# Kernel optimization log

Hardware: AMD Instinct MI355X
Metric: run time of the kernel (lower is better)

Reference implementation:

```python
import jax, jax.numpy as jnp
import numpy as np


def setup_inputs() -> dict:
    key = jax.random.key(0)
    k1, k2 = jax.random.split(key)
    C, N = 64, 500000
    src = jax.random.normal(k1, (C, N), dtype=jnp.float32)
    index = jax.random.randint(k2, (N,), 0, N, dtype=jnp.int64)
    return {"src": src, "index": index}


def reference(src, index):
    # scatter_max(src, index, dim=-1, out=src):
    #   out[c, k] = max(src[c, k], max_{j: index[j]==k} src[c, j])
    #   argmax[c, k] = source position j achieving the segment max
    #                  (sentinel N if the segment is empty / never updated)
    C, N = src.shape
    index = index.astype(jnp.int32)
    # Segment max over the point axis; empty segments get -inf.
    seg_max = jax.ops.segment_max(src.T, index, num_segments=N).T  # [C, N]
    out = jnp.maximum(src, seg_max)
    # argmax: smallest source position whose value equals the segment max.
    pos = jnp.arange(N, dtype=jnp.int32)
    is_max = src == seg_max[:, index]                       # [C, N]
    cand = jnp.where(is_max, pos[None, :], N).astype(jnp.int32)
    arg_min = jax.ops.segment_min(cand.T, index, num_segments=N).T  # [C, N]
    argmax = jnp.where(seg_max >= src, arg_min, N).astype(jnp.int32)
    return out, argmax
```

## Files before the change

kernel.cpp:

```cpp
#include <hip/hip_runtime.h>
#include <stdint.h>

typedef unsigned int u32;
typedef unsigned long long u64;

__device__ __forceinline__ u32 f2o(float f) {
    u32 u = __float_as_uint(f);
    return (u & 0x80000000u) ? ~u : (u | 0x80000000u);
}
__device__ __forceinline__ float o2f(u32 u) {
    return __uint_as_float((u & 0x80000000u) ? (u & 0x7fffffffu) : ~u);
}

#define TJ 64

__global__ __launch_bounds__(256) void scatter_tr_kernel(
        const float* __restrict__ src, const int* __restrict__ index,
        u64* __restrict__ packt, int N, int vec_ok) {
    __shared__ float tile[64 * 65];
    __shared__ int idx[TJ];
    const int j0 = blockIdx.x * TJ;
    const int t = threadIdx.x;
    const int nj = min(TJ, N - j0);

    if (t < nj) idx[t] = index[j0 + t];

    if (nj == TJ && vec_ok) {
        const int r0 = t >> 4, q = t & 15;
        #pragma unroll
        for (int p = 0; p < 4; ++p) {
            const int c = r0 + p * 16;
            float4 v = *reinterpret_cast<const float4*>(src + (size_t)c * N + j0 + q * 4);
            float* d = &tile[c * 65 + q * 4];
            d[0] = v.x; d[1] = v.y; d[2] = v.z; d[3] = v.w;
        }
    } else {
        for (int e = t; e < 64 * TJ; e += 256) {
            const int c = e >> 6, jj = e & 63;
            tile[c * 65 + jj] = (jj < nj) ? src[(size_t)c * N + j0 + jj] : 0.0f;
        }
    }
    __syncthreads();

    const int lane = t & 63, w = t >> 6;
    #pragma unroll 4
    for (int jj = w; jj < nj; jj += 4) {
        const int j = j0 + jj;
        const u32 k = (u32)idx[jj];
        const float v = tile[lane * 65 + jj];
        const u64 p = ((u64)f2o(v) << 32) | (u32)(~(u32)j);
        atomicMax(&packt[(size_t)k * 64 + lane], p);
    }
}

__global__ __launch_bounds__(256) void finalize_tr_kernel(
        const float* __restrict__ src, const u64* __restrict__ packt,
        float* __restrict__ outv, float* __restrict__ outa, int N, u32 NV) {
    __shared__ u32 lord[64 * 65];
    __shared__ u32 larg[64 * 65];
    const int k0 = blockIdx.x * 64;
    const int t = threadIdx.x;
    const int nk = min(64, N - k0);

    {
        const u64* base = packt + (size_t)k0 * 64;
        const int npairs = nk * 32;
        #pragma unroll
        for (int v = 0; v < 8; ++v) {
            const int i2 = t + v * 256;
            if (i2 < npairs) {
                const int e = i2 * 2;
                ulonglong2 p = *reinterpret_cast<const ulonglong2*>(base + e);
                const int kk = e >> 6, c = e & 63;
                lord[kk * 65 + c]     = (u32)(p.x >> 32);
                larg[kk * 65 + c]     = ~(u32)p.x;
                lord[kk * 65 + c + 1] = (u32)(p.y >> 32);
                larg[kk * 65 + c + 1] = ~(u32)p.y;
            }
        }
    }
    __syncthreads();

    const int lane = t & 63, w = t >> 6;
    const int q = lane & 15, cg = lane >> 4;
    const int kq = q * 4;
    #pragma unroll
    for (int p = 0; p < 4; ++p) {
        const int c = p * 16 + w * 4 + cg;
        const size_t off = (size_t)c * N + k0 + kq;
        if (kq + 3 < nk) {
            float4 s = *reinterpret_cast<const float4*>(src + off);
            float sv[4] = {s.x, s.y, s.z, s.w};
            float4 ov, av;
            float* po = &ov.x; float* pa = &av.x;
            #pragma unroll
            for (int i = 0; i < 4; ++i) {
                const u32 ord = lord[(kq + i) * 65 + c];
                float o, a;
                if (ord == 0u) { o = sv[i]; a = (float)NV; }
                else {
                    const float m = o2f(ord);
                    o = fmaxf(sv[i], m);
                    a = (m >= sv[i]) ? (float)larg[(kq + i) * 65 + c] : (float)NV;
                }
                po[i] = o; pa[i] = a;
            }
            *reinterpret_cast<float4*>(outv + off) = ov;
            *reinterpret_cast<float4*>(outa + off) = av;
        } else {
            for (int i = 0; i < 4 && kq + i < nk; ++i) {
                const float s = src[off + i];
                const u32 ord = lord[(kq + i) * 65 + c];
                float o, a;
                if (ord == 0u) { o = s; a = (float)NV; }
                else {
                    const float m = o2f(ord);
                    o = fmaxf(s, m);
                    a = (m >= s) ? (float)larg[(kq + i) * 65 + c] : (float)NV;
                }
                outv[off + i] = o;
                outa[off + i] = a;
            }
        }
    }
}

__global__ void scatter_pack_kernel(const float* __restrict__ src,
                                    const int* __restrict__ index,
                                    u64* __restrict__ pack, int N) {
    const int c = blockIdx.y;
    const int j0 = (blockIdx.x * blockDim.x + threadIdx.x) * 4;
    const float* srow = src + (size_t)c * N;
    u64* prow = pack + (size_t)c * N;
    if (j0 + 3 < N) {
        float4 v = *reinterpret_cast<const float4*>(srow + j0);
        int4 k = *reinterpret_cast<const int4*>(index + j0);
        atomicMax(&prow[k.x], ((u64)f2o(v.x) << 32) | (u32)(~(u32)(j0 + 0)));
        atomicMax(&prow[k.y], ((u64)f2o(v.y) << 32) | (u32)(~(u32)(j0 + 1)));
        atomicMax(&prow[k.z], ((u64)f2o(v.z) << 32) | (u32)(~(u32)(j0 + 2)));
        atomicMax(&prow[k.w], ((u64)f2o(v.w) << 32) | (u32)(~(u32)(j0 + 3)));
    } else {
        for (int j = j0; j < N; ++j)
            atomicMax(&prow[index[j]], ((u64)f2o(srow[j]) << 32) | (u32)(~(u32)j));
    }
}

__global__ void finalize_pack_kernel(const float* __restrict__ src,
                                     const u64* __restrict__ pack,
                                     float* __restrict__ outv,
                                     float* __restrict__ outa,
                                     size_t total, u32 NV) {
    size_t i = (size_t)blockIdx.x * blockDim.x + threadIdx.x;
    const size_t stride = (size_t)gridDim.x * blockDim.x;
    for (; i < total; i += stride) {
        const float s = src[i];
        const u64 p = pack[i];
        const u32 ord = (u32)(p >> 32);
        float o, a;
        if (ord == 0u) { o = s; a = (float)NV; }
        else {
            const float m = o2f(ord);
            o = fmaxf(s, m);
            a = (m >= s) ? (float)(~(u32)p) : (float)NV;
        }
        outv[i] = o;
        outa[i] = a;
    }
}

extern "C" void kernel_launch(void* const* d_in, const int* in_sizes, int n_in,
                              void* d_out, int out_size, void* d_ws, size_t ws_size,
                              hipStream_t stream) {
    const float* src = (const float*)d_in[0];
    const int* index = (const int*)d_in[1];
    const int N = in_sizes[1];
    const int C = in_sizes[0] / N;
    const size_t total = (size_t)C * N;
    float* out = (float*)d_out;

    u64* pack = (u64*)d_ws;
    hipMemsetAsync(pack, 0, total * sizeof(u64), stream);

    if (C == 64 && ws_size >= total * sizeof(u64)) {
        const int nblk = (N + TJ - 1) / TJ;
        const int vec_ok = ((N & 3) == 0);
        scatter_tr_kernel<<<nblk, 256, 0, stream>>>(src, index, pack, N, vec_ok);
        finalize_tr_kernel<<<nblk, 256, 0, stream>>>(src, pack, out, out + total,
                                                     N, (u32)N);
    } else {
        const int TPB = 256;
        dim3 sg((N + TPB * 4 - 1) / (TPB * 4), C);
        scatter_pack_kernel<<<sg, TPB, 0, stream>>>(src, index, pack, N);
        finalize_pack_kernel<<<2048, TPB, 0, stream>>>(src, pack, out, out + total,
                                                       total, (u32)N);
    }
}
```

Before: 567.6 us.

## Replace 64-bit atomic scatter-max with counting-sort segment reduction

Replaces the per-element 64-bit atomicMax scatter into a C×N packed buffer with a counting sort of indices (histogram, three-stage prefix scan, scatter into sorted order), followed by a gather-based segmented max over a transposed copy of src. This avoids zeroing and atomically updating a 256 MB packed workspace and the atomic traffic, though it adds several small kernel launches and random row gathers from the transposed src. Ties resolve by the smallest j through the same packed compare.

```diff
diff --git a/kernel.cpp b/kernel.cpp
--- a/kernel.cpp
+++ b/kernel.cpp
@@ -13,6 +13,197 @@
 }
 
 #define TJ 64
+
+
+__global__ __launch_bounds__(256) void transpose_hist_kernel(
+        const float* __restrict__ src, const int* __restrict__ index,
+        float* __restrict__ srct, u32* __restrict__ count, u32* __restrict__ pos,
+        int N, int vec_ok) {
+    __shared__ float tile[64 * 65];
+    __shared__ int idx[TJ];
+    const int j0 = blockIdx.x * TJ;
+    const int t = threadIdx.x;
+    const int nj = min(TJ, N - j0);
+
+    if (t < nj) idx[t] = index[j0 + t];
+
+    if (nj == TJ && vec_ok) {
+        const int r0 = t >> 4, q = t & 15;
+        #pragma unroll
+        for (int p = 0; p < 4; ++p) {
+            const int c = r0 + p * 16;
+            float4 v = *reinterpret_cast<const float4*>(src + (size_t)c * N + j0 + q * 4);
+            float* d = &tile[c * 65 + q * 4];
+            d[0] = v.x; d[1] = v.y; d[2] = v.z; d[3] = v.w;
+        }
+    } else {
+        for (int e = t; e < 64 * TJ; e += 256) {
+            const int c = e >> 6, jj = e & 63;
+            tile[c * 65 + jj] = (jj < nj) ? src[(size_t)c * N + j0 + jj] : 0.0f;
+        }
+    }
+    __syncthreads();
+
+    if (t < nj) pos[j0 + t] = atomicAdd(&count[idx[t]], 1u);
+
+    const int lane = t & 63, w = t >> 6;
+    #pragma unroll 4
+    for (int jj = w; jj < nj; jj += 4) {
+        srct[(size_t)(j0 + jj) * 64 + lane] = tile[lane * 65 + jj];
+    }
+}
+
+__global__ __launch_bounds__(256) void scan_bsum_kernel(
+        const u32* __restrict__ count, u32* __restrict__ bsum, int N) {
+    __shared__ u32 s[256];
+    const int b = blockIdx.x, t = threadIdx.x;
+    const int base = b * 1024 + t * 4;
+    u32 a = 0;
+    if (base + 3 < N) {
+        uint4 v = *reinterpret_cast<const uint4*>(count + base);
+        a = v.x + v.y + v.z + v.w;
+    } else {
+        for (int i = 0; i < 4; ++i) if (base + i < N) a += count[base + i];
+    }
+    s[t] = a; __syncthreads();
+    for (int off = 128; off > 0; off >>= 1) {
+        if (t < off) s[t] += s[t + off];
+        __syncthreads();
+    }
+    if (t == 0) bsum[b] = s[0];
+}
+
+__global__ __launch_bounds__(1024) void scan_top_kernel(
+        const u32* __restrict__ bsum, u32* __restrict__ boffs, int NB) {
+    __shared__ u32 s[1024];
+    const int t = threadIdx.x;
+    const u32 v = (t < NB) ? bsum[t] : 0u;
+    s[t] = v; __syncthreads();
+    for (int off = 1; off < 1024; off <<= 1) {
+        u32 x = (t >= off) ? s[t - off] : 0u;
+        __syncthreads();
+        s[t] += x;
+        __syncthreads();
+    }
+    if (t < NB) boffs[t] = s[t] - v;
+}
+
+__global__ __launch_bounds__(256) void scan_final_kernel(
+        const u32* __restrict__ count, const u32* __restrict__ boffs,
+        u32* __restrict__ offs, int N) {
+    __shared__ u32 s[256];
+    const int b = blockIdx.x, t = threadIdx.x;
+    const int base = b * 1024 + t * 4;
+    u32 a0 = 0, a1 = 0, a2 = 0, a3 = 0;
+    if (base + 3 < N) {
+        uint4 v = *reinterpret_cast<const uint4*>(count + base);
+        a0 = v.x; a1 = v.y; a2 = v.z; a3 = v.w;
+    } else {
+        if (base < N)     a0 = count[base];
+        if (base + 1 < N) a1 = count[base + 1];
+        if (base + 2 < N) a2 = count[base + 2];
+        if (base + 3 < N) a3 = count[base + 3];
+    }
+    const u32 ts = a0 + a1 + a2 + a3;
+    s[t] = ts; __syncthreads();
+    for (int off = 1; off < 256; off <<= 1) {
+        u32 x = (t >= off) ? s[t - off] : 0u;
+        __syncthreads();
+        s[t] += x;
+        __syncthreads();
+    }
+    u32 run = boffs[b] + s[t] - ts;
+    if (base < N)     offs[base] = run;     run += a0;
+    if (base + 1 < N) offs[base + 1] = run; run += a1;
+    if (base + 2 < N) offs[base + 2] = run; run += a2;
+    if (base + 3 < N) offs[base + 3] = run;
+}
+
+__global__ __launch_bounds__(256) void sort_scatter_kernel(
+        const int* __restrict__ index, const u32* __restrict__ pos,
+        const u32* __restrict__ offs, u32* __restrict__ sortedj, int N) {
+    const int j = blockIdx.x * 256 + threadIdx.x;
+    if (j < N) {
+        const int k = index[j];
+        sortedj[offs[k] + pos[j]] = (u32)j;
+    }
+}
+
+__global__ __launch_bounds__(256) void segreduce_finalize_kernel(
+        const float* __restrict__ src, const float* __restrict__ srct,
+        const u32* __restrict__ sortedj, const u32* __restrict__ offs,
+        float* __restrict__ outv, float* __restrict__ outa, int N, u32 NV) {
+    __shared__ u32 lord[64 * 65];
+    __shared__ u32 larg[64 * 65];
+    __shared__ u32 loffs[65];
+    const int k0 = blockIdx.x * 64;
+    const int t = threadIdx.x;
+    const int nk = min(64, N - k0);
+    if (t < 65) {
+        const int ik = k0 + t;
+        loffs[t] = (ik < N) ? offs[ik] : (u32)N;
+    }
+    __syncthreads();
+
+    const int lane = t & 63, w = t >> 6;
+
+    for (int kk = w * 16; kk < w * 16 + 16; ++kk) {
+        if (kk >= nk) break;
+        const u32 s = loffs[kk], e = loffs[kk + 1];
+        u64 pm = 0ull;
+        for (u32 x = s; x < e; ++x) {
+            const u32 jj = sortedj[x];
+            const float v = srct[(size_t)jj * 64 + lane];
+            const u64 p = ((u64)f2o(v) << 32) | (u32)(~jj);
+            pm = pm > p ? pm : p;
+        }
+        lord[kk * 65 + lane] = (u32)(pm >> 32);
+        larg[kk * 65 + lane] = ~(u32)pm;
+    }
+    __syncthreads();
+
+    const int q = lane & 15, cg = lane >> 4;
+    const int kq = q * 4;
+    #pragma unroll
+    for (int p = 0; p < 4; ++p) {
+        const int c = p * 16 + w * 4 + cg;
+        const size_t off = (size_t)c * N + k0 + kq;
+        if (kq + 3 < nk) {
+            float4 sv4 = *reinterpret_cast<const float4*>(src + off);
+            float sv[4] = {sv4.x, sv4.y, sv4.z, sv4.w};
+            float4 ov, av;
+            float* po = &ov.x; float* pa = &av.x;
+            #pragma unroll
+            for (int i = 0; i < 4; ++i) {
+                const u32 ord = lord[(kq + i) * 65 + c];
+                float o, a;
+                if (ord == 0u) { o = sv[i]; a = (float)NV; }
+                else {
+                    const float m = o2f(ord);
+                    o = fmaxf(sv[i], m);
+                    a = (m >= sv[i]) ? (float)larg[(kq + i) * 65 + c] : (float)NV;
+                }
+                po[i] = o; pa[i] = a;
+            }
+            *reinterpret_cast<float4*>(outv + off) = ov;
+            *reinterpret_cast<float4*>(outa + off) = av;
+        } else {
+            for (int i = 0; i < 4 && kq + i < nk; ++i) {
+                const float s = src[off + i];
+                const u32 ord = lord[(kq + i) * 65 + c];
+                float o, a;
+                if (ord == 0u) { o = s; a = (float)NV; }
+                else {
+                    const float m = o2f(ord);
+                    o = fmaxf(s, m);
+                    a = (m >= s) ? (float)larg[(kq + i) * 65 + c] : (float)NV;
+                }
+                outv[off + i] = o;
+                outa[off + i] = a;
+            }
+        }
+    }
+}
 
 __global__ __launch_bounds__(256) void scatter_tr_kernel(
         const float* __restrict__ src, const int* __restrict__ index,
@@ -22,9 +213,7 @@
     const int j0 = blockIdx.x * TJ;
     const int t = threadIdx.x;
     const int nj = min(TJ, N - j0);
-
     if (t < nj) idx[t] = index[j0 + t];
-
     if (nj == TJ && vec_ok) {
         const int r0 = t >> 4, q = t & 15;
         #pragma unroll
@@ -41,7 +230,6 @@
         }
     }
     __syncthreads();
-
     const int lane = t & 63, w = t >> 6;
     #pragma unroll 4
     for (int jj = w; jj < nj; jj += 4) {
@@ -61,7 +249,6 @@
     const int k0 = blockIdx.x * 64;
     const int t = threadIdx.x;
     const int nk = min(64, N - k0);
-
     {
         const u64* base = packt + (size_t)k0 * 64;
         const int npairs = nk * 32;
@@ -80,7 +267,6 @@
         }
     }
     __syncthreads();
-
     const int lane = t & 63, w = t >> 6;
     const int q = lane & 15, cg = lane >> 4;
     const int kq = q * 4;
@@ -178,16 +364,39 @@
     const size_t total = (size_t)C * N;
     float* out = (float*)d_out;
 
-    u64* pack = (u64*)d_ws;
-    hipMemsetAsync(pack, 0, total * sizeof(u64), stream);
-
-    if (C == 64 && ws_size >= total * sizeof(u64)) {
-        const int nblk = (N + TJ - 1) / TJ;
-        const int vec_ok = ((N & 3) == 0);
+    const int NB = (N + 1023) / 1024;
+    float* srct   = (float*)d_ws;
+    u32* count    = (u32*)((char*)d_ws + total * sizeof(float));
+    u32* pos      = count + N;
+    u32* offsa    = pos + N;
+    u32* sortedj  = offsa + N;
+    u32* bsum     = sortedj + N;
+    u32* boffs    = bsum + 1024;
+    const size_t need = total * sizeof(float) + (size_t)N * 4 * sizeof(u32) + 2048 * sizeof(u32);
+
+    const int nblk = (N + TJ - 1) / TJ;
+    const int vec_ok = ((N & 3) == 0);
+
+    if (C == 64 && NB <= 1024 && ws_size >= need) {
+        hipMemsetAsync(count, 0, (size_t)N * sizeof(u32), stream);
+        transpose_hist_kernel<<<nblk, 256, 0, stream>>>(src, index, srct, count, pos,
+                                                        N, vec_ok);
+        scan_bsum_kernel<<<NB, 256, 0, stream>>>(count, bsum, N);
+        scan_top_kernel<<<1, 1024, 0, stream>>>(bsum, boffs, NB);
+        scan_final_kernel<<<NB, 256, 0, stream>>>(count, boffs, offsa, N);
+        sort_scatter_kernel<<<(N + 255) / 256, 256, 0, stream>>>(index, pos, offsa,
+                                                                 sortedj, N);
+        segreduce_finalize_kernel<<<nblk, 256, 0, stream>>>(src, srct, sortedj, offsa,
+                                                            out, out + total, N, (u32)N);
+    } else if (C == 64 && ws_size >= total * sizeof(u64)) {
+        u64* pack = (u64*)d_ws;
+        hipMemsetAsync(pack, 0, total * sizeof(u64), stream);
         scatter_tr_kernel<<<nblk, 256, 0, stream>>>(src, index, pack, N, vec_ok);
         finalize_tr_kernel<<<nblk, 256, 0, stream>>>(src, pack, out, out + total,
                                                      N, (u32)N);
     } else {
+        u64* pack = (u64*)d_ws;
+        hipMemsetAsync(pack, 0, total * sizeof(u64), stream);
         const int TPB = 256;
         dim3 sg((N + TPB * 4 - 1) / (TPB * 4), C);
         scatter_pack_kernel<<<sg, TPB, 0, stream>>>(src, index, pack, N);
```

New measurement: 575.5 us. Within noise of the previous version (+1.4%).
